# Kernel tuning notes

Hardware: AMD Instinct MI355X
Metric: run time of the kernel (lower is better)

## Reference

```python
import jax, jax.numpy as jnp
import numpy as np

B, T, F = 128, 1024, 128
H, A, L = 128, 128, 7


def setup_inputs() -> dict:
    key = jax.random.key(0)
    ks = jax.random.split(key, 10)
    s = 0.1  # init scale
    return {
        "x": jax.random.normal(ks[0], (B, T, F), dtype=jnp.float32),
        "Wih": jax.random.normal(ks[1], (L, 4 * H, F), dtype=jnp.float32) * s,
        "Whh": jax.random.normal(ks[2], (L, 4 * H, H), dtype=jnp.float32) * s,
        "bih": jax.random.normal(ks[3], (L, 4 * H), dtype=jnp.float32) * s,
        "bhh": jax.random.normal(ks[4], (L, 4 * H), dtype=jnp.float32) * s,
        "Wa": jax.random.normal(ks[5], (A, H), dtype=jnp.float32) * s,
        "ba": jax.random.normal(ks[6], (A,), dtype=jnp.float32) * s,
        "Wf": jax.random.normal(ks[7], (1, H), dtype=jnp.float32) * s,
        "bf": jax.random.normal(ks[8], (1,), dtype=jnp.float32) * s,
    }


def _lstm_layer(x, Wih_l, Whh_l, bih_l, bhh_l):
    # x: [B, T, F_in] -> hidden sequence [B, T, H]; PyTorch gate order i,f,g,o.
    b, t, _ = x.shape
    xg = jnp.einsum('bti,gi->btg', x, Wih_l) + bih_l + bhh_l  # [B, T, 4H]

    def step(carry, xg_t):
        h, c = carry
        z = xg_t + h @ Whh_l.T  # [B, 4H]
        i, f, g, o = jnp.split(z, 4, axis=-1)
        c = jax.nn.sigmoid(f) * c + jax.nn.sigmoid(i) * jnp.tanh(g)
        h = jax.nn.sigmoid(o) * jnp.tanh(c)
        return (h, c), h

    h0 = jnp.zeros((b, H), x.dtype)
    (_, _), hs = jax.lax.scan(step, (h0, h0), jnp.swapaxes(xg, 0, 1))
    return jnp.swapaxes(hs, 0, 1)  # [B, T, H]


def reference(x, Wih, Whh, bih, bhh, Wa, ba, Wf, bf):
    out = x
    for l in range(Wih.shape[0]):  # fixed small layer count
        out = _lstm_layer(out, Wih[l], Whh[l], bih[l], bhh[l])
    # attention: softmax over time of tanh(Linear(out))  -> [B, T, A]
    attn = jax.nn.softmax(jnp.tanh(jnp.einsum('bth,ah->bta', out, Wa) + ba), axis=1)
    applied = jnp.einsum('bta,bth->bah', attn, out)  # bmm(attn^T, out): [B, A, H]
    logits = applied[:, -1, :] @ Wf.T + bf  # last attention head row -> [B, 1]
    return jax.nn.sigmoid(logits)
```

## Files before the change

kernel.cpp:

```cpp
#include <hip/hip_runtime.h>
#include <cstdint>
#include <cstddef>

#define DEV __device__ __forceinline__

typedef __attribute__((ext_vector_type(4))) float    f32x4;
typedef __attribute__((ext_vector_type(4))) _Float16 f16x4;
typedef __attribute__((ext_vector_type(8))) _Float16 f16x8;

static constexpr int B_ = 128, T_ = 1024, F_ = 128, H_ = 128, L_ = 7;
static constexpr int M_ = B_ * T_;

DEV float fexp2(float x){
#if __has_builtin(__builtin_amdgcn_exp2f)
  return __builtin_amdgcn_exp2f(x);
#else
  return exp2f(x);
#endif
}
DEV float frcp(float x){
#if __has_builtin(__builtin_amdgcn_rcpf)
  return __builtin_amdgcn_rcpf(x);
#else
  return 1.0f/x;
#endif
}
DEV float fsig(float x){ return frcp(1.f + fexp2(-1.44269504f*x)); }
DEV float ftanh(float x){
  x = fminf(10.f, fmaxf(-10.f, x));
  float e = fexp2(2.88539008f*x);
  return (e - 1.f) * frcp(e + 1.f);
}

__global__ void k_cvt_x(const float4* __restrict__ x4, f16x4* __restrict__ xo, int n4){
  int i = blockIdx.x*blockDim.x + threadIdx.x;
  int stride = gridDim.x*blockDim.x;
  for (; i < n4; i += stride){
    float4 v = x4[i];
    f16x4 o = {(_Float16)v.x, (_Float16)v.y, (_Float16)v.z, (_Float16)v.w};
    xo[i] = o;
  }
}

__global__ void k_cvt_w(const float* __restrict__ Wih, const float* __restrict__ Whh,
                        const float* __restrict__ bih, const float* __restrict__ bhh,
                        _Float16* __restrict__ Wc, float* __restrict__ biasp){
  int idx = blockIdx.x*blockDim.x + threadIdx.x;
  int l    = idx >> 17;
  int rem  = idx & 131071;
  int m    = rem >> 8;
  int k    = rem & 255;
  int gate = m & 3, hrow = m >> 2;
  int srow = l*512 + gate*128 + hrow;
  float v = (k < 128) ? Whh[(size_t)srow*128 + k] : Wih[(size_t)srow*128 + (k-128)];
  Wc[idx] = (_Float16)v;
  if (idx < L_*512){
    int bl = idx >> 9, r = idx & 511;
    int bh = r >> 2, bg = r & 3;
    int s = bl*512 + bg*128 + bh;
    biasp[idx] = bih[s] + bhh[s];
  }
}

__global__ __launch_bounds__(512, 2) void k_recur(
    const _Float16* __restrict__ xcvt,
    _Float16* __restrict__ buf0, _Float16* __restrict__ buf1,
    const _Float16* __restrict__ Wc, const float4* __restrict__ biasp,
    int* __restrict__ flags){
  const int wg = blockIdx.x;
  const int layer = wg >> 3;
  const int g = wg & 7;
  const int tid = threadIdx.x;
  const int w = tid >> 6, l64 = tid & 63;
  const int q = l64 >> 4, i = l64 & 15;

  const _Float16* src = (layer == 0) ? xcvt : (((layer - 1) & 1) ? buf1 : buf0);
  _Float16* dst = (layer & 1) ? buf1 : buf0;

  __shared__ _Float16 hx[2][16][260];

  f16x8 wf[4][8];
  {
    const _Float16* wbase = Wc + ((size_t)layer*512 + i)*256 + 8*q;
#pragma unroll
    for (int mt = 0; mt < 4; ++mt)
#pragma unroll
      for (int kt = 0; kt < 8; ++kt)
        wf[mt][kt] = *(const f16x8*)(wbase + (size_t)(16*(4*w+mt))*256 + 32*kt);
  }
  f32x4 bs[4];
#pragma unroll
  for (int mt = 0; mt < 4; ++mt){
    float4 bv = biasp[layer*128 + 4*(4*w+mt) + q];
    f32x4 t = {bv.x, bv.y, bv.z, bv.w};
    bs[mt] = t;
  }
  float cst[4] = {0.f, 0.f, 0.f, 0.f};

  const int bb = tid >> 5;
  const int cc = tid & 31;
  const size_t srow = ((size_t)(g*16 + bb))*T_*H_;
  const _Float16* xsrc = src + srow + cc*4;
  _Float16*       hdst = dst + srow + cc*4;
  int* fIn  = flags + ((layer - 1)*8 + g)*128;
  int* fOut = flags + (layer*8 + g)*128;

  auto poll = [&](int* p){
    if (tid == 0){
      while (__hip_atomic_load(p, __ATOMIC_ACQUIRE, __HIP_MEMORY_SCOPE_AGENT) == 0)
        __builtin_amdgcn_s_sleep(2);
    }
    __syncthreads();
  };

  if (layer > 0) poll(fIn + 0);
  {
    f16x4 z4 = {(_Float16)0.f, (_Float16)0.f, (_Float16)0.f, (_Float16)0.f};
    *(f16x4*)&hx[0][bb][cc*4] = z4;
    f16x4 x0 = *(const f16x4*)(xsrc);
    *(f16x4*)&hx[0][bb][128 + cc*4] = x0;
  }
  __syncthreads();

  for (int t = 0; t < T_; ++t){
    const int cur = t & 1, nxt = cur ^ 1;
    if (layer > 0 && ((t + 1) & 7) == 0 && (t + 1) < T_) poll(fIn + ((t + 1) >> 3));
    int tp = (t + 1 < T_) ? t + 1 : T_ - 1;
    f16x4 xreg = *(const f16x4*)(xsrc + (size_t)tp*H_);
    f16x4 freg;
    if (t > 0) freg = *(const f16x4*)&hx[cur][bb][cc*4];
    f16x8 bf[8];
#pragma unroll
    for (int kt = 0; kt < 8; ++kt)
      bf[kt] = *(const f16x8*)&hx[cur][i][32*kt + 8*q];
    f32x4 acc[4];
#pragma unroll
    for (int mt = 0; mt < 4; ++mt){
      acc[mt] = bs[mt];
#pragma unroll
      for (int kt = 0; kt < 8; ++kt)
        acc[mt] = __builtin_amdgcn_mfma_f32_16x16x32_f16(wf[mt][kt], bf[kt], acc[mt], 0, 0, 0);
    }
    if (t > 0) *(f16x4*)(hdst + (size_t)(t - 1)*H_) = freg;
#pragma unroll
    for (int mt = 0; mt < 4; ++mt){
      f32x4 z = acc[mt];
      cst[mt] = fsig(z[1])*cst[mt] + fsig(z[0])*ftanh(z[2]);
      float h = fsig(z[3])*ftanh(cst[mt]);
      hx[nxt][i][4*(4*w + mt) + q] = (_Float16)h;
    }
    *(f16x4*)&hx[nxt][bb][128 + cc*4] = xreg;
    asm volatile("s_waitcnt lgkmcnt(0)\n\ts_barrier" ::: "memory");
    if (layer < 6 && t > 0 && (t & 7) == 0){
      asm volatile("s_waitcnt vmcnt(0)" ::: "memory");
      __syncthreads();
      if (tid == 0)
        __hip_atomic_store(fOut + ((t >> 3) - 1), 1, __ATOMIC_RELEASE, __HIP_MEMORY_SCOPE_AGENT);
    }
  }
  {
    f16x4 freg = *(const f16x4*)&hx[0][bb][cc*4];
    *(f16x4*)(hdst + (size_t)(T_ - 1)*H_) = freg;
  }
  if (layer < 6){
    asm volatile("s_waitcnt vmcnt(0)" ::: "memory");
    __syncthreads();
    if (tid == 0)
      __hip_atomic_store(fOut + 127, 1, __ATOMIC_RELEASE, __HIP_MEMORY_SCOPE_AGENT);
  }
}

__global__ __launch_bounds__(256) void k_attn(const _Float16* __restrict__ out,
                                              const float* __restrict__ Wa, const float* __restrict__ ba,
                                              const float* __restrict__ Wf, const float* __restrict__ bfv,
                                              float* __restrict__ y){
  int b = blockIdx.x, tid = threadIdx.x;
  __shared__ float was[H_];
  __shared__ float p[T_];
  __shared__ float red[64];
  __shared__ float app[256];
  if (tid < H_) was[tid] = Wa[127*H_ + tid];
  __syncthreads();
  float bav = ba[127];
  for (int t = tid; t < T_; t += 256){
    const _Float16* row = out + (size_t)(b*T_ + t)*H_;
    float acc = 0.f;
#pragma unroll
    for (int k = 0; k < H_; k += 8){
      f16x8 u = *(const f16x8*)(row + k);
      acc += (float)u[0]*was[k+0] + (float)u[1]*was[k+1]
           + (float)u[2]*was[k+2] + (float)u[3]*was[k+3]
           + (float)u[4]*was[k+4] + (float)u[5]*was[k+5]
           + (float)u[6]*was[k+6] + (float)u[7]*was[k+7];
    }
    p[t] = ftanh(acc + bav);
  }
  __syncthreads();
  float m = -1e30f;
  for (int t = tid; t < T_; t += 256) m = fmaxf(m, p[t]);
  for (int off = 32; off; off >>= 1) m = fmaxf(m, __shfl_xor(m, off));
  if ((tid & 63) == 0) red[tid >> 6] = m;
  __syncthreads();
  if (tid == 0) red[8] = fmaxf(fmaxf(red[0], red[1]), fmaxf(red[2], red[3]));
  __syncthreads();
  float smax = red[8];
  float lsum = 0.f;
  for (int t = tid; t < T_; t += 256){
    float e = fexp2(1.44269504f*(p[t] - smax));
    p[t] = e; lsum += e;
  }
  for (int off = 32; off; off >>= 1) lsum += __shfl_xor(lsum, off);
  if ((tid & 63) == 0) red[16 + (tid >> 6)] = lsum;
  __syncthreads();
  float rden = frcp(red[16] + red[17] + red[18] + red[19]);
  int h = tid & (H_ - 1);
  int half = tid >> 7;
  float acc = 0.f;
  for (int t = half*512; t < half*512 + 512; ++t)
    acc += p[t] * (float)out[(size_t)(b*T_ + t)*H_ + h];
  app[tid] = acc;
  __syncthreads();
  if (tid < H_){
    float applied = (app[tid] + app[tid + H_]) * rden;
    float v = applied * Wf[tid];
    for (int off = 32; off; off >>= 1) v += __shfl_xor(v, off);
    if (tid == 0)  red[32] = v;
    if (tid == 64) red[33] = v;
  }
  __syncthreads();
  if (tid == 0) y[b] = fsig(red[32] + red[33] + bfv[0]);
}

extern "C" void kernel_launch(void* const* d_in, const int* in_sizes, int n_in,
                              void* d_out, int out_size, void* d_ws, size_t ws_size,
                              hipStream_t stream){
  const float* x   = (const float*)d_in[0];
  const float* Wih = (const float*)d_in[1];
  const float* Whh = (const float*)d_in[2];
  const float* bih = (const float*)d_in[3];
  const float* bhh = (const float*)d_in[4];
  const float* Wa  = (const float*)d_in[5];
  const float* ba  = (const float*)d_in[6];
  const float* Wf  = (const float*)d_in[7];
  const float* bfv = (const float*)d_in[8];
  float* y = (float*)d_out;

  char* ws = (char*)d_ws;
  size_t off = 0;
  auto alloc = [&](size_t bytes) -> void* {
    void* p = ws + off; off += (bytes + 255) & ~(size_t)255; return p;
  };
  _Float16* xcvt  = (_Float16*)alloc((size_t)M_*H_*2);
  _Float16* buf0  = (_Float16*)alloc((size_t)M_*H_*2);
  _Float16* buf1  = (_Float16*)alloc((size_t)M_*H_*2);
  _Float16* Wc    = (_Float16*)alloc((size_t)L_*512*256*2);
  float*    biasp = (float*)   alloc((size_t)L_*512*4);
  int*      flags = (int*)     alloc((size_t)6*8*128*4);

  hipMemsetAsync(flags, 0, (size_t)6*8*128*4, stream);
  k_cvt_x<<<2048, 256, 0, stream>>>((const float4*)x, (f16x4*)xcvt, M_*F_/4);
  k_cvt_w<<<3584, 256, 0, stream>>>(Wih, Whh, bih, bhh, Wc, biasp);
  k_recur<<<56, 512, 0, stream>>>(xcvt, buf0, buf1, Wc, (const float4*)biasp, flags);
  k_attn<<<128, 256, 0, stream>>>(buf0, Wa, ba, Wf, bfv, y);
}
```

Measured before the change: 1.358 ms.

## Split recurrent GEMM into hidden and input parts, precompute input projection a step ahead

The per-step K=256 MFMA chain is split into an h·Whh part on the critical path and an x·Wih part computed one step ahead into double-buffered accumulators. The input rows go through a 4-deep LDS ring with register prefetch, and the loop is unrolled by two. Weight rows are re-permuted so each lane writes a packed f16x4 of h, and tanh becomes a cheaper sigmoid form. Flag atomics switch to relaxed ordering, outputs use nontemporal stores, and polling moves earlier. Relaxed atomics may weaken cross-workgroup visibility guarantees, and the extra registers and LDS may reduce occupancy.

After: 1.614 ms. 18.9% more time.

```diff
diff --git a/kernel.cpp b/kernel.cpp
--- a/kernel.cpp
+++ b/kernel.cpp
@@ -10,6 +10,7 @@
 
 static constexpr int B_ = 128, T_ = 1024, F_ = 128, H_ = 128, L_ = 7;
 static constexpr int M_ = B_ * T_;
+static constexpr int NCH = 128;
 
 DEV float fexp2(float x){
 #if __has_builtin(__builtin_amdgcn_exp2f)
@@ -26,11 +27,8 @@
 #endif
 }
 DEV float fsig(float x){ return frcp(1.f + fexp2(-1.44269504f*x)); }
-DEV float ftanh(float x){
-  x = fminf(10.f, fmaxf(-10.f, x));
-  float e = fexp2(2.88539008f*x);
-  return (e - 1.f) * frcp(e + 1.f);
-}
+DEV float ftanh(float x){ return 2.f*frcp(1.f + fexp2(-2.88539008f*x)) - 1.f; }
+DEV void  ntst4(_Float16* p, f16x4 v){ __builtin_nontemporal_store(v, (f16x4*)p); }
 
 __global__ void k_cvt_x(const float4* __restrict__ x4, f16x4* __restrict__ xo, int n4){
   int i = blockIdx.x*blockDim.x + threadIdx.x;
@@ -44,28 +42,32 @@
 
 __global__ void k_cvt_w(const float* __restrict__ Wih, const float* __restrict__ Whh,
                         const float* __restrict__ bih, const float* __restrict__ bhh,
-                        _Float16* __restrict__ Wc, float* __restrict__ biasp){
+                        _Float16* __restrict__ Wc, float* __restrict__ biasc){
   int idx = blockIdx.x*blockDim.x + threadIdx.x;
   int l    = idx >> 17;
   int rem  = idx & 131071;
-  int m    = rem >> 8;
+  int m2   = rem >> 8;
   int k    = rem & 255;
-  int gate = m & 3, hrow = m >> 2;
-  int srow = l*512 + gate*128 + hrow;
+  int w  = m2 >> 6;
+  int mt = (m2 >> 4) & 3;
+  int q  = (m2 >> 2) & 3;
+  int r  = m2 & 3;
+  int hrow = 16*w + 4*q + mt;
+  int srow = l*512 + r*128 + hrow;
   float v = (k < 128) ? Whh[(size_t)srow*128 + k] : Wih[(size_t)srow*128 + (k-128)];
   Wc[idx] = (_Float16)v;
   if (idx < L_*512){
-    int bl = idx >> 9, r = idx & 511;
-    int bh = r >> 2, bg = r & 3;
-    int s = bl*512 + bg*128 + bh;
-    biasp[idx] = bih[s] + bhh[s];
-  }
-}
-
-__global__ __launch_bounds__(512, 2) void k_recur(
+    int bl = idx >> 9, bm = idx & 511;
+    int bw = bm >> 6, bmt = (bm >> 4) & 3, bq = (bm >> 2) & 3, br = bm & 3;
+    int bs = bl*512 + br*128 + (16*bw + 4*bq + bmt);
+    biasc[idx] = bih[bs] + bhh[bs];
+  }
+}
+
+__global__ __launch_bounds__(512) void k_wave(
     const _Float16* __restrict__ xcvt,
     _Float16* __restrict__ buf0, _Float16* __restrict__ buf1,
-    const _Float16* __restrict__ Wc, const float4* __restrict__ biasp,
+    const _Float16* __restrict__ Wc, const float4* __restrict__ biasc,
     int* __restrict__ flags){
   const int wg = blockIdx.x;
   const int layer = wg >> 3;
@@ -77,23 +79,26 @@
   const _Float16* src = (layer == 0) ? xcvt : (((layer - 1) & 1) ? buf1 : buf0);
   _Float16* dst = (layer & 1) ? buf1 : buf0;
 
-  __shared__ _Float16 hx[2][16][260];
-
-  f16x8 wf[4][8];
+  __shared__ _Float16 hx[2][16][132];
+  __shared__ _Float16 xb[4][16][132];
+
+  f16x8 wfH[4][4], wfX[4][4];
   {
-    const _Float16* wbase = Wc + ((size_t)layer*512 + i)*256 + 8*q;
+    const _Float16* wbase = Wc + ((size_t)(layer*512) + 64*w + i)*256 + 8*q;
 #pragma unroll
     for (int mt = 0; mt < 4; ++mt)
 #pragma unroll
-      for (int kt = 0; kt < 8; ++kt)
-        wf[mt][kt] = *(const f16x8*)(wbase + (size_t)(16*(4*w+mt))*256 + 32*kt);
-  }
-  f32x4 bs[4];
+      for (int kt = 0; kt < 4; ++kt){
+        wfH[mt][kt] = *(const f16x8*)(wbase + (size_t)(16*mt)*256 + 32*kt);
+        wfX[mt][kt] = *(const f16x8*)(wbase + (size_t)(16*mt)*256 + 128 + 32*kt);
+      }
+  }
+  f32x4 bias[4];
 #pragma unroll
   for (int mt = 0; mt < 4; ++mt){
-    float4 bv = biasp[layer*128 + 4*(4*w+mt) + q];
+    float4 bv = biasc[layer*128 + 16*w + 4*mt + q];
     f32x4 t = {bv.x, bv.y, bv.z, bv.w};
-    bs[mt] = t;
+    bias[mt] = t;
   }
   float cst[4] = {0.f, 0.f, 0.f, 0.f};
 
@@ -102,12 +107,12 @@
   const size_t srow = ((size_t)(g*16 + bb))*T_*H_;
   const _Float16* xsrc = src + srow + cc*4;
   _Float16*       hdst = dst + srow + cc*4;
-  int* fIn  = flags + ((layer - 1)*8 + g)*128;
-  int* fOut = flags + (layer*8 + g)*128;
+  int* fIn  = flags + ((layer > 0 ? layer - 1 : 0)*8 + g)*NCH;
+  int* fOut = flags + (layer*8 + g)*NCH;
 
   auto poll = [&](int* p){
     if (tid == 0){
-      while (__hip_atomic_load(p, __ATOMIC_ACQUIRE, __HIP_MEMORY_SCOPE_AGENT) == 0)
+      while (__hip_atomic_load(p, __ATOMIC_RELAXED, __HIP_MEMORY_SCOPE_AGENT) == 0)
         __builtin_amdgcn_s_sleep(2);
     }
     __syncthreads();
@@ -117,56 +122,110 @@
   {
     f16x4 z4 = {(_Float16)0.f, (_Float16)0.f, (_Float16)0.f, (_Float16)0.f};
     *(f16x4*)&hx[0][bb][cc*4] = z4;
-    f16x4 x0 = *(const f16x4*)(xsrc);
-    *(f16x4*)&hx[0][bb][128 + cc*4] = x0;
-  }
-  __syncthreads();
-
-  for (int t = 0; t < T_; ++t){
-    const int cur = t & 1, nxt = cur ^ 1;
-    if (layer > 0 && ((t + 1) & 7) == 0 && (t + 1) < T_) poll(fIn + ((t + 1) >> 3));
-    int tp = (t + 1 < T_) ? t + 1 : T_ - 1;
-    f16x4 xreg = *(const f16x4*)(xsrc + (size_t)tp*H_);
-    f16x4 freg;
-    if (t > 0) freg = *(const f16x4*)&hx[cur][bb][cc*4];
-    f16x8 bf[8];
-#pragma unroll
-    for (int kt = 0; kt < 8; ++kt)
-      bf[kt] = *(const f16x8*)&hx[cur][i][32*kt + 8*q];
-    f32x4 acc[4];
+    f16x4 r0 = *(const f16x4*)(xsrc);
+    f16x4 r1 = *(const f16x4*)(xsrc + (size_t)H_);
+    f16x4 r2 = *(const f16x4*)(xsrc + (size_t)2*H_);
+    *(f16x4*)&xb[0][bb][cc*4] = r0;
+    *(f16x4*)&xb[1][bb][cc*4] = r1;
+    *(f16x4*)&xb[2][bb][cc*4] = r2;
+  }
+  f16x4 xn0 = *(const f16x4*)(xsrc + (size_t)3*H_);
+  f16x4 xn1 = *(const f16x4*)(xsrc + (size_t)4*H_);
+  __syncthreads();
+
+  f32x4 xzA[4], xzB[4];
+  {
+    f16x8 b0[4], b1[4];
+#pragma unroll
+    for (int kt = 0; kt < 4; ++kt){
+      b0[kt] = *(const f16x8*)&xb[0][i][32*kt + 8*q];
+      b1[kt] = *(const f16x8*)&xb[1][i][32*kt + 8*q];
+    }
 #pragma unroll
     for (int mt = 0; mt < 4; ++mt){
-      acc[mt] = bs[mt];
-#pragma unroll
-      for (int kt = 0; kt < 8; ++kt)
-        acc[mt] = __builtin_amdgcn_mfma_f32_16x16x32_f16(wf[mt][kt], bf[kt], acc[mt], 0, 0, 0);
-    }
-    if (t > 0) *(f16x4*)(hdst + (size_t)(t - 1)*H_) = freg;
-#pragma unroll
-    for (int mt = 0; mt < 4; ++mt){
-      f32x4 z = acc[mt];
-      cst[mt] = fsig(z[1])*cst[mt] + fsig(z[0])*ftanh(z[2]);
-      float h = fsig(z[3])*ftanh(cst[mt]);
-      hx[nxt][i][4*(4*w + mt) + q] = (_Float16)h;
-    }
-    *(f16x4*)&hx[nxt][bb][128 + cc*4] = xreg;
-    asm volatile("s_waitcnt lgkmcnt(0)\n\ts_barrier" ::: "memory");
+      xzA[mt] = bias[mt]; xzB[mt] = bias[mt];
+#pragma unroll
+      for (int kt = 0; kt < 4; ++kt){
+        xzA[mt] = __builtin_amdgcn_mfma_f32_16x16x32_f16(wfX[mt][kt], b0[kt], xzA[mt], 0, 0, 0);
+        xzB[mt] = __builtin_amdgcn_mfma_f32_16x16x32_f16(wfX[mt][kt], b1[kt], xzB[mt], 0, 0, 0);
+      }
+    }
+  }
+
+#define BODY(XZ, CUR, TT)                                                        \
+  {                                                                              \
+    f16x4 freg;                                                                  \
+    if ((TT) > 0) freg = *(const f16x4*)&hx[CUR][bb][cc*4];                      \
+    f16x8 bf[4], bx[4];                                                          \
+    _Pragma("unroll")                                                            \
+    for (int kt = 0; kt < 4; ++kt)                                               \
+      bf[kt] = *(const f16x8*)&hx[CUR][i][32*kt + 8*q];                          \
+    {                                                                            \
+      const _Float16* xrow = &xb[((TT) + 2) & 3][i][8*q];                        \
+      _Pragma("unroll")                                                          \
+      for (int kt = 0; kt < 4; ++kt)                                             \
+        bx[kt] = *(const f16x8*)(xrow + 32*kt);                                  \
+    }                                                                            \
+    f32x4 acc[4];                                                                \
+    _Pragma("unroll")                                                            \
+    for (int mt = 0; mt < 4; ++mt) acc[mt] = XZ[mt];                             \
+    _Pragma("unroll")                                                            \
+    for (int kt = 0; kt < 4; ++kt){                                              \
+      acc[0] = __builtin_amdgcn_mfma_f32_16x16x32_f16(wfH[0][kt], bf[kt], acc[0], 0, 0, 0); \
+      acc[1] = __builtin_amdgcn_mfma_f32_16x16x32_f16(wfH[1][kt], bf[kt], acc[1], 0, 0, 0); \
+      acc[2] = __builtin_amdgcn_mfma_f32_16x16x32_f16(wfH[2][kt], bf[kt], acc[2], 0, 0, 0); \
+      acc[3] = __builtin_amdgcn_mfma_f32_16x16x32_f16(wfH[3][kt], bf[kt], acc[3], 0, 0, 0); \
+    }                                                                            \
+    if ((TT) > 0) ntst4(hdst + (size_t)((TT) - 1)*H_, freg);                     \
+    *(f16x4*)&xb[((TT) + 3) & 3][bb][cc*4] = xn0;                                \
+    xn0 = xn1;                                                                   \
+    { int rp = (TT) + 5; if (rp > T_ - 1) rp = T_ - 1;                           \
+      xn1 = *(const f16x4*)(xsrc + (size_t)rp*H_); }                             \
+    f16x4 hv;                                                                    \
+    _Pragma("unroll")                                                            \
+    for (int mt = 0; mt < 4; ++mt){                                              \
+      f32x4 z = acc[mt];                                                         \
+      float si = fsig(z[0]), sf = fsig(z[1]);                                    \
+      float gt = ftanh(z[2]);                                                    \
+      float so = fsig(z[3]);                                                     \
+      cst[mt] = sf*cst[mt] + si*gt;                                              \
+      hv[mt] = (_Float16)(so * ftanh(cst[mt]));                                  \
+    }                                                                            \
+    *(f16x4*)&hx[(CUR) ^ 1][i][16*w + 4*q] = hv;                                 \
+    _Pragma("unroll")                                                            \
+    for (int mt = 0; mt < 4; ++mt) XZ[mt] = bias[mt];                            \
+    _Pragma("unroll")                                                            \
+    for (int kt = 0; kt < 4; ++kt){                                              \
+      XZ[0] = __builtin_amdgcn_mfma_f32_16x16x32_f16(wfX[0][kt], bx[kt], XZ[0], 0, 0, 0); \
+      XZ[1] = __builtin_amdgcn_mfma_f32_16x16x32_f16(wfX[1][kt], bx[kt], XZ[1], 0, 0, 0); \
+      XZ[2] = __builtin_amdgcn_mfma_f32_16x16x32_f16(wfX[2][kt], bx[kt], XZ[2], 0, 0, 0); \
+      XZ[3] = __builtin_amdgcn_mfma_f32_16x16x32_f16(wfX[3][kt], bx[kt], XZ[3], 0, 0, 0); \
+    }                                                                            \
+    asm volatile("s_waitcnt lgkmcnt(0)\n\ts_barrier" ::: "memory");              \
+  }
+
+  for (int t = 0; t < T_; t += 2){
+    BODY(xzA, 0, t)
     if (layer < 6 && t > 0 && (t & 7) == 0){
       asm volatile("s_waitcnt vmcnt(0)" ::: "memory");
       __syncthreads();
       if (tid == 0)
-        __hip_atomic_store(fOut + ((t >> 3) - 1), 1, __ATOMIC_RELEASE, __HIP_MEMORY_SCOPE_AGENT);
-    }
-  }
+        __hip_atomic_store(fOut + ((t >> 3) - 1), 1, __ATOMIC_RELAXED, __HIP_MEMORY_SCOPE_AGENT);
+    }
+    if (layer > 0 && ((t + 6) & 7) == 0 && (t + 6) < T_) poll(fIn + ((t + 6) >> 3));
+    BODY(xzB, 1, t + 1)
+  }
+#undef BODY
+
   {
     f16x4 freg = *(const f16x4*)&hx[0][bb][cc*4];
-    *(f16x4*)(hdst + (size_t)(T_ - 1)*H_) = freg;
+    ntst4(hdst + (size_t)(T_ - 1)*H_, freg);
   }
   if (layer < 6){
     asm volatile("s_waitcnt vmcnt(0)" ::: "memory");
     __syncthreads();
     if (tid == 0)
-      __hip_atomic_store(fOut + 127, 1, __ATOMIC_RELEASE, __HIP_MEMORY_SCOPE_AGENT);
+      __hip_atomic_store(fOut + (NCH - 1), 1, __ATOMIC_RELAXED, __HIP_MEMORY_SCOPE_AGENT);
   }
 }
 
@@ -254,12 +313,12 @@
   _Float16* buf0  = (_Float16*)alloc((size_t)M_*H_*2);
   _Float16* buf1  = (_Float16*)alloc((size_t)M_*H_*2);
   _Float16* Wc    = (_Float16*)alloc((size_t)L_*512*256*2);
-  float*    biasp = (float*)   alloc((size_t)L_*512*4);
-  int*      flags = (int*)     alloc((size_t)6*8*128*4);
-
-  hipMemsetAsync(flags, 0, (size_t)6*8*128*4, stream);
+  float*    biasc = (float*)   alloc((size_t)L_*512*4);
+  int*      flags = (int*)     alloc((size_t)L_*8*NCH*4);
+
+  hipMemsetAsync(flags, 0, (size_t)L_*8*NCH*4, stream);
   k_cvt_x<<<2048, 256, 0, stream>>>((const float4*)x, (f16x4*)xcvt, M_*F_/4);
-  k_cvt_w<<<3584, 256, 0, stream>>>(Wih, Whh, bih, bhh, Wc, biasp);
-  k_recur<<<56, 512, 0, stream>>>(xcvt, buf0, buf1, Wc, (const float4*)biasp, flags);
+  k_cvt_w<<<3584, 256, 0, stream>>>(Wih, Whh, bih, bhh, Wc, biasc);
+  k_wave<<<56, 512, 0, stream>>>(xcvt, buf0, buf1, Wc, (const float4*)biasc, flags);
   k_attn<<<128, 256, 0, stream>>>(buf0, Wa, ba, Wf, bfv, y);
 }
```
